# Kernel optimization log

Hardware: AMD Instinct MI355X
Metric: run time of the kernel (lower is better)

The kernel has to match this reference:

```python
import jax, jax.numpy as jnp
import numpy as np
import math

V, T, E, N = 32000, 128, 64, 1024
SIGMA_MIN, SIGMA_MAX, C = 0.1, 10.0, 2.0


def setup_inputs() -> dict:
    key = jax.random.key(0)
    k1, k2, k3, k4, k5 = jax.random.split(key, 5)
    return {
        "x": jax.random.normal(k1, (T, N), dtype=jnp.float32),
        "mu": jax.random.normal(k2, (V, E), dtype=jnp.float32),
        "log_sigma": jax.random.normal(k3, (V, E), dtype=jnp.float32),
        "mu_c": jax.random.normal(k4, (T, E), dtype=jnp.float32),
        "log_sigma_c": jax.random.normal(k5, (T, E), dtype=jnp.float32),
        "t": 0,
    }


def reference(x, mu, log_sigma, mu_c, log_sigma_c, t):
    # parameter clamping done in-place in the torch forward
    bound = math.sqrt(C)
    mu = jnp.clip(mu, -bound, bound)
    mu_c = jnp.clip(mu_c, -bound, bound)
    log_sigma = jnp.clip(log_sigma, math.log(SIGMA_MIN), math.log(SIGMA_MAX))
    log_sigma_c = jnp.clip(log_sigma_c, math.log(SIGMA_MIN), math.log(SIGMA_MAX))

    sigma = jnp.exp(log_sigma)        # [V, E]
    sigma_c = jnp.exp(log_sigma_c)    # [T, E]

    # pairwise Gaussian expected-likelihood energy, vectorized over topics
    s = sigma[:, None, :] + sigma_c[None, :, :]            # [V, T, E]
    det_fac = jnp.sum(jnp.log(s), axis=-1)                 # [V, T]
    diff = mu[:, None, :] - mu_c[None, :, :]               # [V, T, E]
    diff_mu = jnp.sum(diff * diff / s, axis=-1)            # [V, T]
    emb_dim = mu.shape[-1]
    log_el = -0.5 * (det_fac + diff_mu + emb_dim * math.log(2.0 * math.pi))

    # per-topic softmax over the vocab axis
    w = jax.nn.softmax(log_el, axis=0)                     # [V, T]

    return w @ x.reshape(-1, x.shape[-1])                  # [V, N]
```

## Files before the change

### kernel.cpp

```cpp
#include <hip/hip_runtime.h>
#include <math.h>

#define VV 32000
#define TT 128
#define EE 64
#define NN 1024
#define NPART 500

static constexpr float BOUND    = 1.41421356237309515f;
static constexpr float LOG_SMIN = -2.30258509299404568f;
static constexpr float LOG_SMAX =  2.30258509299404568f;
static constexpr float LN2      =  0.69314718055994531f;
static constexpr float E_LOG2PI =  64.0f * 1.83787706640934548f;

typedef __attribute__((ext_vector_type(2)))  float f32x2;
typedef __attribute__((ext_vector_type(8)))  short short8;
typedef __attribute__((ext_vector_type(16))) float float16;

static __device__ inline unsigned short f2bf(float f) {
    union { float f; unsigned u; } v; v.f = f;
    unsigned r = v.u + 0x7FFFu + ((v.u >> 16) & 1u);
    return (unsigned short)(r >> 16);
}

__global__ __launch_bounds__(256) void prep_xpose(const float* __restrict__ mu_c,
                                                  const float* __restrict__ log_sigma_c,
                                                  const float* __restrict__ x,
                                                  float* __restrict__ sc,
                                                  float* __restrict__ mc,
                                                  unsigned short* __restrict__ xT) {
    const int tid = threadIdx.x;
    if (blockIdx.x < 32) {
        int i = blockIdx.x * 256 + tid;
        if (i < TT * EE) {
            float ls = log_sigma_c[i];
            ls = fminf(fmaxf(ls, LOG_SMIN), LOG_SMAX);
            sc[i] = __expf(ls);
            float m = mu_c[i];
            mc[i] = fminf(fmaxf(m, -BOUND), BOUND);
        }
    } else {
        const int b = blockIdx.x - 32;
        const int n = b * 128 + (tid & 127);
        const int th = tid >> 7;
        const float* __restrict__ xp = x + n;
#pragma unroll
        for (int i = 0; i < 64; i += 2) {
            int t = th * 64 + i;
            float x0 = xp[(size_t)t * NN];
            float x1 = xp[(size_t)(t + 1) * NN];
            *(unsigned*)&xT[n * TT + t] = (unsigned)f2bf(x0) | ((unsigned)f2bf(x1) << 16);
        }
    }
}

__global__ __launch_bounds__(256) void logits_kernel(const float* __restrict__ mu,
                                                     const float* __restrict__ log_sigma,
                                                     const float* __restrict__ sc,
                                                     const float* __restrict__ mc,
                                                     float* __restrict__ logitsT,
                                                     float* __restrict__ pm,
                                                     float* __restrict__ pl) {
    __shared__ float part[16][4][64];
    const int tid  = threadIdx.x;
    const int lane = tid & 63;
    const int wv   = tid >> 6;
    const int v0   = blockIdx.x * 64;
    const int t0   = blockIdx.y * 32;
    const int e0u  = __builtin_amdgcn_readfirstlane(wv) * 16;

    f32x2 sv[8], mv[8];
    {
        const float* __restrict__ lsp = log_sigma + (size_t)(v0 + lane) * EE + e0u;
        const float* __restrict__ mup = mu        + (size_t)(v0 + lane) * EE + e0u;
#pragma unroll
        for (int j = 0; j < 8; j++) {
            float a = lsp[2 * j], b = lsp[2 * j + 1];
            a = fminf(fmaxf(a, LOG_SMIN), LOG_SMAX);
            b = fminf(fmaxf(b, LOG_SMIN), LOG_SMAX);
            sv[j] = f32x2{__expf(a), __expf(b)};
            float c = mup[2 * j], d = mup[2 * j + 1];
            mv[j] = f32x2{fminf(fmaxf(c, -BOUND), BOUND), fminf(fmaxf(d, -BOUND), BOUND)};
        }
    }

    f32x2 cs[2][8], cm[2][8];
    {
        const f32x2* __restrict__ sp = (const f32x2*)(sc + t0 * EE + e0u);
        const f32x2* __restrict__ mp = (const f32x2*)(mc + t0 * EE + e0u);
#pragma unroll
        for (int j = 0; j < 8; j++) { cs[0][j] = sp[j]; cm[0][j] = mp[j]; }
    }

    for (int tb = 0; tb < 2; tb++) {
#pragma unroll
        for (int i = 0; i < 16; i++) {
            const int ti  = tb * 16 + i;
            const int cur = ti & 1;
            if (ti < 31) {
                const int tn = t0 + ti + 1;
                const f32x2* __restrict__ sp = (const f32x2*)(sc + tn * EE + e0u);
                const f32x2* __restrict__ mp = (const f32x2*)(mc + tn * EE + e0u);
#pragma unroll
                for (int j = 0; j < 8; j++) { cs[cur ^ 1][j] = sp[j]; cm[cur ^ 1][j] = mp[j]; }
            }
            f32x2 q = {0.f, 0.f};
            f32x2 p = {1.f, 1.f};
#pragma unroll
            for (int j = 0; j < 8; j++) {
                f32x2 s = sv[j] + cs[cur][j];
                p *= s;
                f32x2 d = mv[j] - cm[cur][j];
                f32x2 r;
                r.x = __builtin_amdgcn_rcpf(s.x);
                r.y = __builtin_amdgcn_rcpf(s.y);
                q += d * d * r;
            }
            part[i][wv][lane] = __log2f(p.x * p.y) * LN2 + q.x + q.y;
        }
        __syncthreads();
#pragma unroll
        for (int k = 0; k < 4; k++) {
            const int i = wv * 4 + k;
            const int t = t0 + tb * 16 + i;
            float sum = part[i][0][lane] + part[i][1][lane] + part[i][2][lane] + part[i][3][lane];
            float logit = -0.5f * (sum + E_LOG2PI);
            logitsT[t * VV + v0 + lane] = logit;

            float m = logit;
#pragma unroll
            for (int off = 1; off < 64; off <<= 1) m = fmaxf(m, __shfl_xor(m, off));
            float sx = __expf(logit - m);
#pragma unroll
            for (int off = 1; off < 64; off <<= 1) sx += __shfl_xor(sx, off);
            if (lane == 0) {
                pm[t * NPART + blockIdx.x] = m;
                pl[t * NPART + blockIdx.x] = sx;
            }
        }
        __syncthreads();
    }
}

__global__ __launch_bounds__(256) void merge_stats(const float* __restrict__ pm,
                                                   const float* __restrict__ pl,
                                                   float* __restrict__ stats) {
    const int tid = threadIdx.x;
    const int t = blockIdx.x;
    __shared__ float red[8];
    float m = -3.4e38f;
    for (int j = tid; j < NPART; j += 256) m = fmaxf(m, pm[t * NPART + j]);
#pragma unroll
    for (int off = 1; off < 64; off <<= 1) m = fmaxf(m, __shfl_xor(m, off));
    if ((tid & 63) == 0) red[tid >> 6] = m;
    __syncthreads();
    m = fmaxf(fmaxf(red[0], red[1]), fmaxf(red[2], red[3]));

    float l = 0.0f;
    for (int j = tid; j < NPART; j += 256)
        l += pl[t * NPART + j] * __expf(pm[t * NPART + j] - m);
#pragma unroll
    for (int off = 1; off < 64; off <<= 1) l += __shfl_xor(l, off);
    if ((tid & 63) == 0) red[4 + (tid >> 6)] = l;
    __syncthreads();
    if (tid == 0) {
        float tot = red[4] + red[5] + red[6] + red[7];
        stats[t] = m;
        stats[TT + t] = 1.0f / tot;
    }
}

__global__ __launch_bounds__(256) void make_w(const float* __restrict__ logitsT,
                                              const float* __restrict__ stats,
                                              unsigned short* __restrict__ w) {
    __shared__ __attribute__((aligned(16))) unsigned short wl[64][136];
    __shared__ float sl[256];
    const int tid = threadIdx.x;
    const int v0 = blockIdx.x * 64;

    sl[tid] = stats[tid];
    __syncthreads();

    {
        const int v = tid & 63;
        const int tg = tid >> 6;
        const float* __restrict__ lp = logitsT + v0 + v;
#pragma unroll
        for (int i = 0; i < 32; i += 2) {
            int t = tg * 32 + i;
            float lg0 = lp[(size_t)t * VV];
            float lg1 = lp[(size_t)(t + 1) * VV];
            float w0 = __expf(lg0 - sl[t])     * sl[TT + t];
            float w1 = __expf(lg1 - sl[t + 1]) * sl[TT + t + 1];
            *(unsigned*)&wl[v][t] = (unsigned)f2bf(w0) | ((unsigned)f2bf(w1) << 16);
        }
    }
    __syncthreads();

    {
        const int v = tid >> 2;
        const int seg = (tid & 3) * 32;
#pragma unroll
        for (int j = 0; j < 4; j++) {
            uint4 d = *(const uint4*)&wl[v][seg + j * 8];
            *(uint4*)&w[(size_t)(v0 + v) * TT + seg + j * 8] = d;
        }
    }
}

__global__ __launch_bounds__(256) void wx_mfma(const unsigned short* __restrict__ w,
                                               const unsigned short* __restrict__ xT,
                                               float* __restrict__ out) {
    const int tid = threadIdx.x;
    const int n0 = blockIdx.x * 128;
    const int v0 = blockIdx.y * 64;
    const int lane = tid & 63;
    const int wv   = tid >> 6;
    const int vh   = (wv & 1) * 32;
    const int nh   = (wv >> 1) * 64;
    const int r32  = lane & 31;
    const int koff = (lane >> 5) * 8;

    const unsigned short* __restrict__ ap  = w  + (size_t)(v0 + vh + r32) * TT + koff;
    const unsigned short* __restrict__ bp0 = xT + (size_t)(n0 + nh + r32) * TT + koff;
    const unsigned short* __restrict__ bp1 = bp0 + 32 * TT;

    float16 acc0 = {0,0,0,0,0,0,0,0,0,0,0,0,0,0,0,0};
    float16 acc1 = {0,0,0,0,0,0,0,0,0,0,0,0,0,0,0,0};
#pragma unroll
    for (int kb = 0; kb < 8; kb++) {
        short8 a  = *(const short8*)(ap  + kb * 16);
        short8 b0 = *(const short8*)(bp0 + kb * 16);
        short8 b1 = *(const short8*)(bp1 + kb * 16);
        acc0 = __builtin_amdgcn_mfma_f32_32x32x16_bf16(a, b0, acc0, 0, 0, 0);
        acc1 = __builtin_amdgcn_mfma_f32_32x32x16_bf16(a, b1, acc1, 0, 0, 0);
    }

    const int col = lane & 31;
    const int rbase = 4 * (lane >> 5);
#pragma unroll
    for (int r = 0; r < 16; r++) {
        int row = (r & 3) + 8 * (r >> 2) + rbase;
        float* dst = out + (size_t)(v0 + vh + row) * NN + n0 + nh + col;
        dst[0]  = acc0[r];
        dst[32] = acc1[r];
    }
}

extern "C" void kernel_launch(void* const* d_in, const int* in_sizes, int n_in,
                              void* d_out, int out_size, void* d_ws, size_t ws_size,
                              hipStream_t stream) {
    const float* x           = (const float*)d_in[0];
    const float* mu          = (const float*)d_in[1];
    const float* log_sigma   = (const float*)d_in[2];
    const float* mu_c        = (const float*)d_in[3];
    const float* log_sigma_c = (const float*)d_in[4];
    float* out = (float*)d_out;

    float* ws      = (float*)d_ws;
    float* logitsT = ws;
    float* pm      = logitsT + (size_t)TT * VV;
    float* pl      = pm + (size_t)TT * NPART;
    float* stats   = pl + (size_t)TT * NPART;
    float* sc      = stats + 2 * TT;
    float* mc      = sc + TT * EE;
    unsigned short* w_bf16 = (unsigned short*)(mc + TT * EE);
    unsigned short* xT     = w_bf16 + (size_t)VV * TT;

    prep_xpose<<<40, 256, 0, stream>>>(mu_c, log_sigma_c, x, sc, mc, xT);
    logits_kernel<<<dim3(VV / 64, 4), 256, 0, stream>>>(mu, log_sigma, sc, mc,
                                                        logitsT, pm, pl);
    merge_stats<<<TT, 256, 0, stream>>>(pm, pl, stats);
    make_w<<<VV / 64, 256, 0, stream>>>(logitsT, stats, w_bf16);
    wx_mfma<<<dim3(NN / 128, VV / 64), 256, 0, stream>>>(w_bf16, xT, out);
}
```

Before: 244.5 us.

## Fuse softmax normalization into the MFMA GEMM and drop the make_w kernel

Removes the separate make_w pass, which wrote a bf16 weight matrix. The GEMM kernel now reads the fp32 logits directly, applies exp2 with a folded per-topic offset (log-sum-exp merged into one constant), and packs to bf16 with a hardware convert instruction. This saves one kernel launch and a write-then-read round trip of the weight matrix. In exchange each of the 8 N-tile blocks recomputes the exponentials and reads the fp32 logits with strided per-k loads, and bf16 packing switches to the hardware rounding. The x transpose prep is also retiled to use more blocks.

```diff
diff --git a/kernel.cpp b/kernel.cpp
--- a/kernel.cpp
+++ b/kernel.cpp
@@ -11,6 +11,7 @@
 static constexpr float LOG_SMIN = -2.30258509299404568f;
 static constexpr float LOG_SMAX =  2.30258509299404568f;
 static constexpr float LN2      =  0.69314718055994531f;
+static constexpr float LOG2E    =  1.44269504088896340f;
 static constexpr float E_LOG2PI =  64.0f * 1.83787706640934548f;
 
 typedef __attribute__((ext_vector_type(2)))  float f32x2;
@@ -21,6 +22,12 @@
     union { float f; unsigned u; } v; v.f = f;
     unsigned r = v.u + 0x7FFFu + ((v.u >> 16) & 1u);
     return (unsigned short)(r >> 16);
+}
+
+static __device__ inline unsigned pack_bf16(float a, float b) {
+    unsigned r;
+    asm("v_cvt_pk_bf16_f32 %0, %1, %2" : "=v"(r) : "v"(a), "v"(b));
+    return r;
 }
 
 __global__ __launch_bounds__(256) void prep_xpose(const float* __restrict__ mu_c,
@@ -41,12 +48,12 @@
         }
     } else {
         const int b = blockIdx.x - 32;
-        const int n = b * 128 + (tid & 127);
-        const int th = tid >> 7;
+        const int n = b * 32 + (tid & 31);
+        const int th = tid >> 5;
         const float* __restrict__ xp = x + n;
 #pragma unroll
-        for (int i = 0; i < 64; i += 2) {
-            int t = th * 64 + i;
+        for (int i = 0; i < 16; i += 2) {
+            int t = th * 16 + i;
             float x0 = xp[(size_t)t * NN];
             float x1 = xp[(size_t)(t + 1) * NN];
             *(unsigned*)&xT[n * TT + t] = (unsigned)f2bf(x0) | ((unsigned)f2bf(x1) << 16);
@@ -165,50 +172,12 @@
     __syncthreads();
     if (tid == 0) {
         float tot = red[4] + red[5] + red[6] + red[7];
-        stats[t] = m;
-        stats[TT + t] = 1.0f / tot;
-    }
-}
-
-__global__ __launch_bounds__(256) void make_w(const float* __restrict__ logitsT,
-                                              const float* __restrict__ stats,
-                                              unsigned short* __restrict__ w) {
-    __shared__ __attribute__((aligned(16))) unsigned short wl[64][136];
-    __shared__ float sl[256];
-    const int tid = threadIdx.x;
-    const int v0 = blockIdx.x * 64;
-
-    sl[tid] = stats[tid];
-    __syncthreads();
-
-    {
-        const int v = tid & 63;
-        const int tg = tid >> 6;
-        const float* __restrict__ lp = logitsT + v0 + v;
-#pragma unroll
-        for (int i = 0; i < 32; i += 2) {
-            int t = tg * 32 + i;
-            float lg0 = lp[(size_t)t * VV];
-            float lg1 = lp[(size_t)(t + 1) * VV];
-            float w0 = __expf(lg0 - sl[t])     * sl[TT + t];
-            float w1 = __expf(lg1 - sl[t + 1]) * sl[TT + t + 1];
-            *(unsigned*)&wl[v][t] = (unsigned)f2bf(w0) | ((unsigned)f2bf(w1) << 16);
-        }
-    }
-    __syncthreads();
-
-    {
-        const int v = tid >> 2;
-        const int seg = (tid & 3) * 32;
-#pragma unroll
-        for (int j = 0; j < 4; j++) {
-            uint4 d = *(const uint4*)&wl[v][seg + j * 8];
-            *(uint4*)&w[(size_t)(v0 + v) * TT + seg + j * 8] = d;
-        }
-    }
-}
-
-__global__ __launch_bounds__(256) void wx_mfma(const unsigned short* __restrict__ w,
+        stats[t] = -(__log2f(tot) + m * LOG2E);
+    }
+}
+
+__global__ __launch_bounds__(256) void wx_mfma(const float* __restrict__ logitsT,
+                                               const float* __restrict__ stats,
                                                const unsigned short* __restrict__ xT,
                                                float* __restrict__ out) {
     const int tid = threadIdx.x;
@@ -221,19 +190,32 @@
     const int r32  = lane & 31;
     const int koff = (lane >> 5) * 8;
 
-    const unsigned short* __restrict__ ap  = w  + (size_t)(v0 + vh + r32) * TT + koff;
+    const float* __restrict__ lp = logitsT + (size_t)koff * VV + v0 + vh + r32;
+    const float* __restrict__ cp = stats + koff;
     const unsigned short* __restrict__ bp0 = xT + (size_t)(n0 + nh + r32) * TT + koff;
     const unsigned short* __restrict__ bp1 = bp0 + 32 * TT;
 
     float16 acc0 = {0,0,0,0,0,0,0,0,0,0,0,0,0,0,0,0};
     float16 acc1 = {0,0,0,0,0,0,0,0,0,0,0,0,0,0,0,0};
-#pragma unroll
+#pragma unroll 2
     for (int kb = 0; kb < 8; kb++) {
-        short8 a  = *(const short8*)(ap  + kb * 16);
+        float lg[8], c[8];
+#pragma unroll
+        for (int j = 0; j < 8; j++) {
+            lg[j] = lp[(size_t)(kb * 16 + j) * VV];
+            c[j]  = cp[kb * 16 + j];
+        }
+        union { short8 v; unsigned u[4]; } a;
+#pragma unroll
+        for (int j = 0; j < 4; j++) {
+            float w0 = exp2f(fmaf(lg[2 * j],     LOG2E, c[2 * j]));
+            float w1 = exp2f(fmaf(lg[2 * j + 1], LOG2E, c[2 * j + 1]));
+            a.u[j] = pack_bf16(w0, w1);
+        }
         short8 b0 = *(const short8*)(bp0 + kb * 16);
         short8 b1 = *(const short8*)(bp1 + kb * 16);
-        acc0 = __builtin_amdgcn_mfma_f32_32x32x16_bf16(a, b0, acc0, 0, 0, 0);
-        acc1 = __builtin_amdgcn_mfma_f32_32x32x16_bf16(a, b1, acc1, 0, 0, 0);
+        acc0 = __builtin_amdgcn_mfma_f32_32x32x16_bf16(a.v, b0, acc0, 0, 0, 0);
+        acc1 = __builtin_amdgcn_mfma_f32_32x32x16_bf16(a.v, b1, acc1, 0, 0, 0);
     }
 
     const int col = lane & 31;
@@ -262,15 +244,13 @@
     float* pm      = logitsT + (size_t)TT * VV;
     float* pl      = pm + (size_t)TT * NPART;
     float* stats   = pl + (size_t)TT * NPART;
-    float* sc      = stats + 2 * TT;
+    float* sc      = stats + TT;
     float* mc      = sc + TT * EE;
-    unsigned short* w_bf16 = (unsigned short*)(mc + TT * EE);
-    unsigned short* xT     = w_bf16 + (size_t)VV * TT;
-
-    prep_xpose<<<40, 256, 0, stream>>>(mu_c, log_sigma_c, x, sc, mc, xT);
+    unsigned short* xT = (unsigned short*)(mc + TT * EE);
+
+    prep_xpose<<<64, 256, 0, stream>>>(mu_c, log_sigma_c, x, sc, mc, xT);
     logits_kernel<<<dim3(VV / 64, 4), 256, 0, stream>>>(mu, log_sigma, sc, mc,
                                                         logitsT, pm, pl);
     merge_stats<<<TT, 256, 0, stream>>>(pm, pl, stats);
-    make_w<<<VV / 64, 256, 0, stream>>>(logitsT, stats, w_bf16);
-    wx_mfma<<<dim3(NN / 128, VV / 64), 256, 0, stream>>>(w_bf16, xT, out);
-}
+    wx_mfma<<<dim3(NN / 128, VV / 64), 256, 0, stream>>>(logitsT, stats, xT, out);
+}
```

Result: slower. 257.7 us (+5.4%).
